# Kernel optimization log

Hardware: AMD Instinct MI355X
Metric: run time of the kernel (lower is better)

The kernel has to match this reference:

```python
import jax, jax.numpy as jnp
import numpy as np

N_NODES = 20000
N_EDGES = 320000
NFEAT = 50
ALPHA = 0.2  # leaky relu slope
EPS = 1e-16


def _gat_head(x, src, dst, W, a, concat):
    # x: (N, Fin), W: (Fin, Fout), a: (2*Fout,)
    N = x.shape[0]
    Wh = x @ W                      # (N, Fout)
    Fout = W.shape[1]
    # edge_h @ a == Wh[src] @ a[:Fout] + Wh[dst] @ a[Fout:]
    s_src = Wh @ a[:Fout]           # (N,)
    s_dst = Wh @ a[Fout:]           # (N,)
    e = jax.nn.leaky_relu(s_src[src] + s_dst[dst], negative_slope=ALPHA)  # (E,)
    # segment softmax over incoming edges of each target node
    e_max = jax.ops.segment_max(e, dst, num_segments=N)   # (N,)
    e_exp = jnp.exp(e - e_max[dst])                         # (E,)
    e_sum = jax.ops.segment_sum(e_exp, dst, num_segments=N)
    att = e_exp / (e_sum[dst] + EPS)                        # (E,)
    msg = Wh[src] * att[:, None]                            # (E, Fout)
    h = jax.ops.segment_sum(msg, dst, num_segments=N)       # (N, Fout)
    return jax.nn.elu(h) if concat else h


def _multi_head(x, src, dst, W, a, concat):
    # W: (H, Fin, Fout), a: (H, 2*Fout) -> (H, N, Fout)
    return jax.vmap(_gat_head, in_axes=(None, None, None, 0, 0, None))(x, src, dst, W, a, concat)


def setup_inputs() -> dict:
    key = jax.random.key(0)
    ks = jax.random.split(key, 8)
    x = jax.random.normal(ks[0], (N_NODES, NFEAT), dtype=jnp.float32)
    edge_index = jax.random.randint(ks[1], (2, N_EDGES), 0, N_NODES, dtype=jnp.int64)
    s = 0.1
    W1 = jax.random.normal(ks[2], (4, NFEAT, 256), dtype=jnp.float32) * s
    a1 = jax.random.normal(ks[3], (4, 512), dtype=jnp.float32) * s
    W2 = jax.random.normal(ks[4], (4, 1024, 256), dtype=jnp.float32) * s
    a2 = jax.random.normal(ks[5], (4, 512), dtype=jnp.float32) * s
    W3 = jax.random.normal(ks[6], (6, 1024, 121), dtype=jnp.float32) * s
    a3 = jax.random.normal(ks[7], (6, 242), dtype=jnp.float32) * s
    return {"x": x, "edge_index": edge_index, "W1": W1, "a1": a1, "W2": W2, "a2": a2, "W3": W3, "a3": a3}


def reference(x, edge_index, W1, a1, W2, a2, W3, a3):
    src, dst = edge_index[0], edge_index[1]
    N = x.shape[0]
    # layer 1: 4 heads, concat -> (N, 1024), then elu
    h1 = _multi_head(x, src, dst, W1, a1, True)      # (4, N, 256)
    x1 = jnp.transpose(h1, (1, 0, 2)).reshape(N, -1)  # concat along feature dim
    x1 = jax.nn.elu(x1)
    # layer 2: 4 heads, concat + skip connection, then elu
    h2 = _multi_head(x1, src, dst, W2, a2, True)
    x2 = jnp.transpose(h2, (1, 0, 2)).reshape(N, -1)
    x2 = jax.nn.elu(x2 + x1)
    # layer 3: 6 heads, no concat-elu, mean over heads
    h3 = _multi_head(x2, src, dst, W3, a3, False)     # (6, N, 121)
    x3 = jnp.mean(h3, axis=0)
    return jax.nn.sigmoid(x3)
```

## Files before the change

kernel.cpp:

```cpp
#include <hip/hip_runtime.h>
#include <cstdint>

#define N_NODES 20000
#define N_EDGES 320000
#define ALPHA 0.2f
#define GAT_EPS 1e-16f
#define MPAD 20096
#define RBLK 157
#define RHI 20
#define SCAN_BLKS 80
#define BT_ROWS 1152

typedef __attribute__((ext_vector_type(8))) _Float16 half8;
typedef __attribute__((ext_vector_type(4))) _Float16 half4t;
typedef __attribute__((ext_vector_type(16))) float f32x16;
typedef __attribute__((ext_vector_type(2))) float f32x2;

__device__ __forceinline__ float elu1(float x) { return x > 0.f ? x : __expf(x) - 1.f; }

__device__ __forceinline__ unsigned char f2fp8(float x) {
    return (unsigned char)(__builtin_amdgcn_cvt_pk_fp8_f32(x, 0.f, 0, false) & 0xff);
}

__device__ __forceinline__ void async16(const void* g, void* l) {
    __builtin_amdgcn_global_load_lds(
        (const __attribute__((address_space(1))) unsigned int*)g,
        (__attribute__((address_space(3))) unsigned int*)l, 16, 0, 0);
}

__global__ void hist_kernel(const int* __restrict__ dst, int* __restrict__ counts, int E) {
    int e = blockIdx.x * blockDim.x + threadIdx.x;
    if (e < E) atomicAdd(&counts[dst[e]], 1);
}

__global__ void scan1_kernel(const int* __restrict__ counts, int* __restrict__ excl,
                             int* __restrict__ partial, int N) {
    __shared__ int sh[256];
    int t = threadIdx.x, b = blockIdx.x;
    int i = b * 256 + t;
    int v = (i < N) ? counts[i] : 0;
    sh[t] = v;
    __syncthreads();
    for (int d = 1; d < 256; d <<= 1) {
        int x = (t >= d) ? sh[t - d] : 0;
        __syncthreads();
        sh[t] += x;
        __syncthreads();
    }
    if (i < N) excl[i] = sh[t] - v;
    if (t == 255) partial[b] = sh[255];
}

__global__ void scan2_kernel(int* __restrict__ partial) {
    __shared__ int sh[128];
    int t = threadIdx.x;
    int v = (t < SCAN_BLKS) ? partial[t] : 0;
    sh[t] = v;
    __syncthreads();
    for (int d = 1; d < 128; d <<= 1) {
        int x = (t >= d) ? sh[t - d] : 0;
        __syncthreads();
        sh[t] += x;
        __syncthreads();
    }
    if (t < SCAN_BLKS) partial[t] = sh[t] - v;
}

__global__ void scan3_kernel(const int* __restrict__ excl, const int* __restrict__ partial,
                             int* __restrict__ rowptr, int* __restrict__ cursor, int N, int E) {
    int t = threadIdx.x, b = blockIdx.x;
    int i = b * 256 + t;
    if (i < N) {
        int v = excl[i] + partial[b];
        rowptr[i] = v;
        cursor[i] = v;
    }
    if (i == 0) rowptr[N] = E;
}

__global__ void scatter_kernel(const int* __restrict__ src, const int* __restrict__ dst,
                               int* __restrict__ cursor, int* __restrict__ esrc, int E) {
    int e = blockIdx.x * blockDim.x + threadIdx.x;
    if (e < E) {
        int p = atomicAdd(&cursor[dst[e]], 1);
        esrc[p] = src[e];
    }
}

__global__ void pack_x16(const float* __restrict__ x, _Float16* __restrict__ A) {
    int idx = blockIdx.x * 256 + threadIdx.x;
    int r = idx >> 6, c = idx & 63;
    float v = (r < N_NODES && c < 50) ? x[r * 50 + c] : 0.f;
    A[idx] = (_Float16)v;
}

__global__ void pack_bt1(const float* __restrict__ W, _Float16* __restrict__ Bt) {
    int idx = blockIdx.x * 256 + threadIdx.x;
    int c = idx >> 6, k = idx & 63;
    int h = c >> 8, f = c & 255;
    float v = (k < 50) ? W[((size_t)h * 50 + k) * 256 + f] : 0.f;
    Bt[idx] = (_Float16)v;
}

__global__ void pack_bt16(const float* __restrict__ W, _Float16* __restrict__ Bt,
                          int F, int Fpad, int Ctot) {
    int c = blockIdx.y;
    int k = blockIdx.x * blockDim.x + threadIdx.x;
    float v = 0.f;
    if (c < Ctot) {
        int h = c / Fpad, f = c - h * Fpad;
        if (f < F) v = W[(size_t)h * 1024 * F + (size_t)k * F + f];
    }
    Bt[(size_t)c * 1024 + k] = (_Float16)v;
}

__global__ __launch_bounds__(64) void wtilde_kernel(const float* __restrict__ W,
                                                    const float* __restrict__ a,
                                                    _Float16* __restrict__ BT, int Kreal,
                                                    int Kdim, int F, int H, int Nfeat) {
    int k = blockIdx.x, j = blockIdx.y;
    if (j >= 2 * H) return;
    int lane = threadIdx.x;
    int h = j < H ? j : j - H;
    int ao = j < H ? 0 : F;
    float s = 0.f;
    if (k < Kreal) {
        const float* wp = W + ((size_t)h * Kreal + k) * F;
        const float* ap = a + (size_t)h * 2 * F + ao;
        for (int f = lane; f < F; f += 64) s += wp[f] * ap[f];
    }
#pragma unroll
    for (int off = 32; off; off >>= 1) s += __shfl_down(s, off);
    if (lane == 0) BT[(size_t)(Nfeat + j) * Kdim + k] = (_Float16)s;
}

__global__ __launch_bounds__(256) void gemm_f16(const _Float16* __restrict__ A,
                                                const _Float16* __restrict__ BT,
                                                unsigned char* __restrict__ C8,
                                                float* __restrict__ SPRE,
                                                int M, int Nfeat, int ld, int Kdim, int Cblk) {
    int id = blockIdx.x;
    int xm = id & 7, q = id >> 3;
    int cb = q % Cblk, rh = q / Cblk;
    int rb = rh * 8 + xm;
    if (rb >= RBLK) return;
    __shared__ __align__(16) _Float16 sA[128 * 64];
    __shared__ __align__(16) _Float16 sB[128 * 64];
    int t = threadIdx.x;
    int row0 = rb * 128, col0 = cb * 128;
    int lane = t & 63, wave = t >> 6;
    int wm = wave >> 1, wn = wave & 1;
    int l31 = lane & 31;
    int lhi = lane >> 5;

    const _Float16* gA = A + (size_t)row0 * Kdim;
    const _Float16* gB = BT + (size_t)col0 * Kdim;

    int sR[4], sgl[4];
#pragma unroll
    for (int i = 0; i < 4; i++) {
        int m = i * 256 + t;
        sR[i] = m >> 3;
        sgl[i] = (m & 7) ^ (sR[i] & 7);
    }

    f32x16 acc[2][2] = {};

    for (int k0 = 0; k0 < Kdim; k0 += 64) {
        __syncthreads();
#pragma unroll
        for (int i = 0; i < 4; i++) {
            const _Float16* pa = gA + (size_t)sR[i] * Kdim + k0 + sgl[i] * 8;
            const _Float16* pb = gB + (size_t)sR[i] * Kdim + k0 + sgl[i] * 8;
            async16(pa, sA + (i * 256 + t) * 8);
            async16(pb, sB + (i * 256 + t) * 8);
        }
        __syncthreads();
#pragma unroll
        for (int kk = 0; kk < 4; kk++) {
            int g = kk * 2 + lhi;
            half8 af[2], bf[2];
#pragma unroll
            for (int mt = 0; mt < 2; mt++) {
                int R = wm * 64 + mt * 32 + l31;
                int gp = g ^ (R & 7);
                af[mt] = *(const half8*)(sA + R * 64 + gp * 8);
            }
#pragma unroll
            for (int nt = 0; nt < 2; nt++) {
                int R = wn * 64 + nt * 32 + l31;
                int gp = g ^ (R & 7);
                bf[nt] = *(const half8*)(sB + R * 64 + gp * 8);
            }
#pragma unroll
            for (int mt = 0; mt < 2; mt++)
#pragma unroll
                for (int nt = 0; nt < 2; nt++)
                    acc[mt][nt] = __builtin_amdgcn_mfma_f32_32x32x16_f16(af[mt], bf[nt], acc[mt][nt], 0, 0, 0);
        }
    }

    int cb32 = col0 + wn * 64 + l31;
    int rb32 = row0 + wm * 64 + 4 * lhi;
#pragma unroll
    for (int mt = 0; mt < 2; mt++)
#pragma unroll
        for (int nt = 0; nt < 2; nt++) {
            int gc = cb32 + nt * 32;
            if (gc < Nfeat) {
#pragma unroll
                for (int r = 0; r < 16; r++) {
                    int gr = rb32 + mt * 32 + (r & 3) + 8 * (r >> 2);
                    if (gr < M) C8[(size_t)gr * ld + gc] = f2fp8(acc[mt][nt][r]);
                }
            } else if (gc < Nfeat + 12) {
                int j = gc - Nfeat;
#pragma unroll
                for (int r = 0; r < 16; r++) {
                    int gr = rb32 + mt * 32 + (r & 3) + 8 * (r >> 2);
                    if (gr < M) SPRE[(size_t)j * N_NODES + gr] = acc[mt][nt][r];
                }
            }
        }
}

__global__ void att_kernel(const int* __restrict__ rowptr,
                           const int* __restrict__ esrc,
                           const float* __restrict__ SS,
                           const float* __restrict__ SD,
                           float* __restrict__ ATT, int N, int H) {
    int n = blockIdx.x;
    int h = threadIdx.x >> 6;
    int lane = threadIdx.x & 63;
    if (h >= H) return;
    int start = rowptr[n], end = rowptr[n + 1];
    const float* ss = SS + (size_t)h * N;
    float sd = SD[(size_t)h * N + n];
    float* att = ATT + (size_t)h * N_EDGES;
    float m = -1e30f, s = 0.f;
    for (int e = start + lane; e < end; e += 64) {
        float sc = ss[esrc[e]] + sd;
        sc = sc > 0.f ? sc : ALPHA * sc;
        float mn = fmaxf(m, sc);
        s = s * __expf(m - mn) + __expf(sc - mn);
        m = mn;
    }
#pragma unroll
    for (int off = 1; off < 64; off <<= 1) {
        float mo = __shfl_xor(m, off);
        float so = __shfl_xor(s, off);
        float mn = fmaxf(m, mo);
        s = s * __expf(m - mn) + so * __expf(mo - mn);
        m = mn;
    }
    float inv = 1.f / (s + GAT_EPS);
    for (int e = start + lane; e < end; e += 64) {
        float sc = ss[esrc[e]] + sd;
        sc = sc > 0.f ? sc : ALPHA * sc;
        att[e] = __expf(sc - m) * inv;
    }
}

__global__ __launch_bounds__(64) void agg256_kernel(const unsigned char* __restrict__ WH8,
                                                    const int* __restrict__ rowptr,
                                                    const int* __restrict__ esrc,
                                                    const float* __restrict__ ATT,
                                                    _Float16* __restrict__ X16,
                                                    int use_skip, int N) {
    int id = blockIdx.x;
    int h = id & 3, n = id >> 2;
    int lane = threadIdx.x;
    int base = h * 256 + lane * 4;
    int start = rowptr[n], end = rowptr[n + 1];
    const float* ap = ATT + (size_t)h * N_EDGES;
    const unsigned char* W = WH8 + base;
    float a0 = 0.f, a1 = 0.f, a2 = 0.f, a3 = 0.f;
    int e = start;
    for (; e + 8 <= end; e += 8) {
#pragma unroll
        for (int u = 0; u < 8; u += 4) {
            int i0 = esrc[e + u], i1 = esrc[e + u + 1], i2 = esrc[e + u + 2], i3 = esrc[e + u + 3];
            float p0 = ap[e + u], p1 = ap[e + u + 1], p2 = ap[e + u + 2], p3 = ap[e + u + 3];
            unsigned int w0 = *(const unsigned int*)(W + (size_t)i0 * 1024);
            unsigned int w1 = *(const unsigned int*)(W + (size_t)i1 * 1024);
            unsigned int w2 = *(const unsigned int*)(W + (size_t)i2 * 1024);
            unsigned int w3 = *(const unsigned int*)(W + (size_t)i3 * 1024);
            f32x2 l0 = __builtin_amdgcn_cvt_pk_f32_fp8((int)w0, false);
            f32x2 h0v = __builtin_amdgcn_cvt_pk_f32_fp8((int)w0, true);
            f32x2 l1 = __builtin_amdgcn_cvt_pk_f32_fp8((int)w1, false);
            f32x2 h1v = __builtin_amdgcn_cvt_pk_f32_fp8((int)w1, true);
            f32x2 l2 = __builtin_amdgcn_cvt_pk_f32_fp8((int)w2, false);
            f32x2 h2v = __builtin_amdgcn_cvt_pk_f32_fp8((int)w2, true);
            f32x2 l3 = __builtin_amdgcn_cvt_pk_f32_fp8((int)w3, false);
            f32x2 h3v = __builtin_amdgcn_cvt_pk_f32_fp8((int)w3, true);
            a0 += p0 * l0.x + p1 * l1.x + p2 * l2.x + p3 * l3.x;
            a1 += p0 * l0.y + p1 * l1.y + p2 * l2.y + p3 * l3.y;
            a2 += p0 * h0v.x + p1 * h1v.x + p2 * h2v.x + p3 * h3v.x;
            a3 += p0 * h0v.y + p1 * h1v.y + p2 * h2v.y + p3 * h3v.y;
        }
    }
    for (; e < end; e++) {
        float p = ap[e];
        unsigned int w = *(const unsigned int*)(W + (size_t)esrc[e] * 1024);
        f32x2 lo = __builtin_amdgcn_cvt_pk_f32_fp8((int)w, false);
        f32x2 hi = __builtin_amdgcn_cvt_pk_f32_fp8((int)w, true);
        a0 += p * lo.x; a1 += p * lo.y; a2 += p * hi.x; a3 += p * hi.y;
    }
    size_t o = (size_t)n * 1024 + base;
    float v0, v1, v2, v3;
    if (use_skip) {
        half4t sk = *(const half4t*)(X16 + o);
        v0 = elu1(elu1(a0) + (float)sk.x);
        v1 = elu1(elu1(a1) + (float)sk.y);
        v2 = elu1(elu1(a2) + (float)sk.z);
        v3 = elu1(elu1(a3) + (float)sk.w);
    } else {
        v0 = elu1(elu1(a0)); v1 = elu1(elu1(a1));
        v2 = elu1(elu1(a2)); v3 = elu1(elu1(a3));
    }
    half4t r;
    r.x = (_Float16)v0; r.y = (_Float16)v1; r.z = (_Float16)v2; r.w = (_Float16)v3;
    *(half4t*)(X16 + o) = r;
}

__global__ __launch_bounds__(128) void agg726_kernel(const unsigned char* __restrict__ WH8,
                                                     const int* __restrict__ rowptr,
                                                     const int* __restrict__ esrc,
                                                     const float* __restrict__ ATT,
                                                     float* __restrict__ out, int N) {
    __shared__ float part[2][124];
    int t = threadIdx.x, n = blockIdx.x;
    int lane = t & 63, wv = t >> 6;
    int h0 = wv * 3;
    int start = rowptr[n], end = rowptr[n + 1];
    float acc[3][2] = {};
    if (lane < 62) {
        const unsigned char* W0 = WH8 + (h0 + 0) * 124 + 2 * lane;
        const unsigned char* W1 = WH8 + (h0 + 1) * 124 + 2 * lane;
        const unsigned char* W2 = WH8 + (h0 + 2) * 124 + 2 * lane;
        const float* ap0 = ATT + (size_t)(h0 + 0) * N_EDGES;
        const float* ap1 = ATT + (size_t)(h0 + 1) * N_EDGES;
        const float* ap2 = ATT + (size_t)(h0 + 2) * N_EDGES;
        int e = start;
        for (; e + 2 <= end; e += 2) {
            size_t sa = (size_t)esrc[e] * 768, sb = (size_t)esrc[e + 1] * 768;
            float pa0 = ap0[e], pa1 = ap1[e], pa2 = ap2[e];
            float pb0 = ap0[e + 1], pb1 = ap1[e + 1], pb2 = ap2[e + 1];
            unsigned short wa0 = *(const unsigned short*)(W0 + sa);
            unsigned short wa1 = *(const unsigned short*)(W1 + sa);
            unsigned short wa2 = *(const unsigned short*)(W2 + sa);
            unsigned short wb0 = *(const unsigned short*)(W0 + sb);
            unsigned short wb1 = *(const unsigned short*)(W1 + sb);
            unsigned short wb2 = *(const unsigned short*)(W2 + sb);
            f32x2 fa0 = __builtin_amdgcn_cvt_pk_f32_fp8((int)wa0, false);
            f32x2 fa1 = __builtin_amdgcn_cvt_pk_f32_fp8((int)wa1, false);
            f32x2 fa2 = __builtin_amdgcn_cvt_pk_f32_fp8((int)wa2, false);
            f32x2 fb0 = __builtin_amdgcn_cvt_pk_f32_fp8((int)wb0, false);
            f32x2 fb1 = __builtin_amdgcn_cvt_pk_f32_fp8((int)wb1, false);
            f32x2 fb2 = __builtin_amdgcn_cvt_pk_f32_fp8((int)wb2, false);
            acc[0][0] += pa0 * fa0.x + pb0 * fb0.x;
            acc[0][1] += pa0 * fa0.y + pb0 * fb0.y;
            acc[1][0] += pa1 * fa1.x + pb1 * fb1.x;
            acc[1][1] += pa1 * fa1.y + pb1 * fb1.y;
            acc[2][0] += pa2 * fa2.x + pb2 * fb2.x;
            acc[2][1] += pa2 * fa2.y + pb2 * fb2.y;
        }
        for (; e < end; e++) {
            size_t sa = (size_t)esrc[e] * 768;
            float p0 = ap0[e], p1 = ap1[e], p2 = ap2[e];
            f32x2 f0 = __builtin_amdgcn_cvt_pk_f32_fp8((int)*(const unsigned short*)(W0 + sa), false);
            f32x2 f1 = __builtin_amdgcn_cvt_pk_f32_fp8((int)*(const unsigned short*)(W1 + sa), false);
            f32x2 f2 = __builtin_amdgcn_cvt_pk_f32_fp8((int)*(const unsigned short*)(W2 + sa), false);
            acc[0][0] += p0 * f0.x; acc[0][1] += p0 * f0.y;
            acc[1][0] += p1 * f1.x; acc[1][1] += p1 * f1.y;
            acc[2][0] += p2 * f2.x; acc[2][1] += p2 * f2.y;
        }
        part[wv][2 * lane]     = acc[0][0] + acc[1][0] + acc[2][0];
        part[wv][2 * lane + 1] = acc[0][1] + acc[1][1] + acc[2][1];
    }
    __syncthreads();
    if (t < 121) {
        float tot = (part[0][t] + part[1][t]) * (1.f / 6.f);
        out[(size_t)n * 121 + t] = 1.f / (1.f + __expf(-tot));
    }
}

extern "C" void kernel_launch(void* const* d_in, const int* in_sizes, int n_in,
                              void* d_out, int out_size, void* d_ws, size_t ws_size,
                              hipStream_t stream) {
    const float* x  = (const float*)d_in[0];
    const int*   ei = (const int*)d_in[1];
    const float* W1 = (const float*)d_in[2];
    const float* a1 = (const float*)d_in[3];
    const float* W2 = (const float*)d_in[4];
    const float* a2 = (const float*)d_in[5];
    const float* W3 = (const float*)d_in[6];
    const float* a3 = (const float*)d_in[7];
    float* out = (float*)d_out;
    const int N = N_NODES, E = N_EDGES;
    const int* src = ei;
    const int* dst = ei + E;

    char* ws = (char*)d_ws;
    size_t off = 0;
    auto alloc = [&](size_t b) { size_t o = off; off += (b + 255) & ~(size_t)255; return o; };
    _Float16* X16  = (_Float16*)(ws + alloc((size_t)MPAD * 1024 * 2));
    unsigned char* WH8 = (unsigned char*)(ws + alloc((size_t)MPAD * 1024));
    _Float16* BT16 = (_Float16*)(ws + alloc((size_t)BT_ROWS * 1024 * 2));
    _Float16* A1   = (_Float16*)(ws + alloc((size_t)MPAD * 64 * 2));
    _Float16* BT1  = (_Float16*)(ws + alloc((size_t)BT_ROWS * 64 * 2));
    float* SPRE   = (float*)(ws + alloc((size_t)12 * N * 4));
    float* ATT    = (float*)(ws + alloc((size_t)6 * E * 4));
    int*   rowptr = (int*)(ws + alloc((size_t)(N + 1) * 4));
    int*   cursor = (int*)(ws + alloc((size_t)N * 4));
    int*   counts = (int*)(ws + alloc((size_t)N * 4));
    int*   excl   = (int*)(ws + alloc((size_t)N * 4));
    int*   partial= (int*)(ws + alloc((size_t)SCAN_BLKS * 4));
    int*   esrc   = (int*)(ws + alloc((size_t)E * 4));

    hipMemsetAsync(counts, 0, (size_t)N * 4, stream);
    hist_kernel<<<(E + 255) / 256, 256, 0, stream>>>(dst, counts, E);
    scan1_kernel<<<SCAN_BLKS, 256, 0, stream>>>(counts, excl, partial, N);
    scan2_kernel<<<1, 128, 0, stream>>>(partial);
    scan3_kernel<<<SCAN_BLKS, 256, 0, stream>>>(excl, partial, rowptr, cursor, N, E);
    scatter_kernel<<<(E + 255) / 256, 256, 0, stream>>>(src, dst, cursor, esrc, E);
    hipMemsetAsync(X16 + (size_t)N * 1024, 0, (size_t)(MPAD - N) * 1024 * 2, stream);

    pack_x16<<<MPAD * 64 / 256, 256, 0, stream>>>(x, A1);
    pack_bt1<<<1024 * 64 / 256, 256, 0, stream>>>(W1, BT1);
    wtilde_kernel<<<dim3(64, 8), 64, 0, stream>>>(W1, a1, BT1, 50, 64, 256, 4, 1024);
    gemm_f16<<<8 * RHI * 9, 256, 0, stream>>>(A1, BT1, WH8, SPRE, N, 1024, 1024, 64, 9);
    att_kernel<<<N, 256, 0, stream>>>(rowptr, esrc, SPRE, SPRE + 4 * N, ATT, N, 4);
    agg256_kernel<<<N * 4, 64, 0, stream>>>(WH8, rowptr, esrc, ATT, X16, 0, N);

    pack_bt16<<<dim3(4, 1024), 256, 0, stream>>>(W2, BT16, 256, 256, 1024);
    wtilde_kernel<<<dim3(1024, 8), 64, 0, stream>>>(W2, a2, BT16, 1024, 1024, 256, 4, 1024);
    gemm_f16<<<8 * RHI * 9, 256, 0, stream>>>(X16, BT16, WH8, SPRE, N, 1024, 1024, 1024, 9);
    att_kernel<<<N, 256, 0, stream>>>(rowptr, esrc, SPRE, SPRE + 4 * N, ATT, N, 4);
    agg256_kernel<<<N * 4, 64, 0, stream>>>(WH8, rowptr, esrc, ATT, X16, 1, N);

    pack_bt16<<<dim3(4, 744), 256, 0, stream>>>(W3, BT16, 121, 124, 744);
    wtilde_kernel<<<dim3(1024, 12), 64, 0, stream>>>(W3, a3, BT16, 1024, 1024, 121, 6, 744);
    gemm_f16<<<8 * RHI * 6, 256, 0, stream>>>(X16, BT16, WH8, SPRE, N, 744, 768, 1024, 6);
    att_kernel<<<N, 384, 0, stream>>>(rowptr, esrc, SPRE, SPRE + 6 * N, ATT, N, 6);
    agg726_kernel<<<N, 128, 0, stream>>>(WH8, rowptr, esrc, ATT, out, N);
}
```

Baseline: 478.4 us.

## Fuse attention softmax into aggregation and double-buffer GEMM LDS tiles

Merges the per-node softmax kernel and the aggregation kernel for all three layers into one kernel. Each wave computes its head's scores, broadcasts the edge indices and weights with readlane, and accumulates the gathered fp8 features, so the ATT edge buffer is no longer written and read back. The GEMM also gains double-buffered LDS with a prefetch of the next K tile issued before compute, removing one barrier per iteration. The risks are the doubled LDS footprint in the GEMM and fewer blocks in the layer-2 aggregation (one block per node instead of one per node and head), which can reduce occupancy. The GEMM prefetch also depends on the barrier at the top of each iteration to keep the async LDS loads and reads in order.

```diff
diff --git a/kernel.cpp b/kernel.cpp
--- a/kernel.cpp
+++ b/kernel.cpp
@@ -26,6 +26,10 @@
     __builtin_amdgcn_global_load_lds(
         (const __attribute__((address_space(1))) unsigned int*)g,
         (__attribute__((address_space(3))) unsigned int*)l, 16, 0, 0);
+}
+
+__device__ __forceinline__ float rdlanef(float v, int j) {
+    return __int_as_float(__builtin_amdgcn_readlane(__float_as_int(v), j));
 }
 
 __global__ void hist_kernel(const int* __restrict__ dst, int* __restrict__ counts, int E) {
@@ -144,8 +148,8 @@
     int cb = q % Cblk, rh = q / Cblk;
     int rb = rh * 8 + xm;
     if (rb >= RBLK) return;
-    __shared__ __align__(16) _Float16 sA[128 * 64];
-    __shared__ __align__(16) _Float16 sB[128 * 64];
+    __shared__ __align__(16) _Float16 sA[2][128 * 64];
+    __shared__ __align__(16) _Float16 sB[2][128 * 64];
     int t = threadIdx.x;
     int row0 = rb * 128, col0 = cb * 128;
     int lane = t & 63, wave = t >> 6;
@@ -166,16 +170,30 @@
 
     f32x16 acc[2][2] = {};
 
+#pragma unroll
+    for (int i = 0; i < 4; i++) {
+        const _Float16* pa = gA + (size_t)sR[i] * Kdim + sgl[i] * 8;
+        const _Float16* pb = gB + (size_t)sR[i] * Kdim + sgl[i] * 8;
+        async16(pa, &sA[0][(i * 256 + t) * 8]);
+        async16(pb, &sB[0][(i * 256 + t) * 8]);
+    }
+
+    int cur = 0;
     for (int k0 = 0; k0 < Kdim; k0 += 64) {
         __syncthreads();
-#pragma unroll
-        for (int i = 0; i < 4; i++) {
-            const _Float16* pa = gA + (size_t)sR[i] * Kdim + k0 + sgl[i] * 8;
-            const _Float16* pb = gB + (size_t)sR[i] * Kdim + k0 + sgl[i] * 8;
-            async16(pa, sA + (i * 256 + t) * 8);
-            async16(pb, sB + (i * 256 + t) * 8);
-        }
-        __syncthreads();
+        int nxt = k0 + 64;
+        if (nxt < Kdim) {
+            int nb = cur ^ 1;
+#pragma unroll
+            for (int i = 0; i < 4; i++) {
+                const _Float16* pa = gA + (size_t)sR[i] * Kdim + nxt + sgl[i] * 8;
+                const _Float16* pb = gB + (size_t)sR[i] * Kdim + nxt + sgl[i] * 8;
+                async16(pa, &sA[nb][(i * 256 + t) * 8]);
+                async16(pb, &sB[nb][(i * 256 + t) * 8]);
+            }
+        }
+        const _Float16* cA = sA[cur];
+        const _Float16* cB = sB[cur];
 #pragma unroll
         for (int kk = 0; kk < 4; kk++) {
             int g = kk * 2 + lhi;
@@ -184,13 +202,13 @@
             for (int mt = 0; mt < 2; mt++) {
                 int R = wm * 64 + mt * 32 + l31;
                 int gp = g ^ (R & 7);
-                af[mt] = *(const half8*)(sA + R * 64 + gp * 8);
+                af[mt] = *(const half8*)(cA + R * 64 + gp * 8);
             }
 #pragma unroll
             for (int nt = 0; nt < 2; nt++) {
                 int R = wn * 64 + nt * 32 + l31;
                 int gp = g ^ (R & 7);
-                bf[nt] = *(const half8*)(sB + R * 64 + gp * 8);
+                bf[nt] = *(const half8*)(cB + R * 64 + gp * 8);
             }
 #pragma unroll
             for (int mt = 0; mt < 2; mt++)
@@ -198,6 +216,7 @@
                 for (int nt = 0; nt < 2; nt++)
                     acc[mt][nt] = __builtin_amdgcn_mfma_f32_32x32x16_f16(af[mt], bf[nt], acc[mt][nt], 0, 0, 0);
         }
+        cur ^= 1;
     }
 
     int cb32 = col0 + wn * 64 + l31;
@@ -224,25 +243,33 @@
         }
 }
 
-__global__ void att_kernel(const int* __restrict__ rowptr,
-                           const int* __restrict__ esrc,
-                           const float* __restrict__ SS,
-                           const float* __restrict__ SD,
-                           float* __restrict__ ATT, int N, int H) {
+__global__ __launch_bounds__(256) void attagg256_kernel(const int* __restrict__ rowptr,
+                                                        const int* __restrict__ esrc,
+                                                        const float* __restrict__ SPRE,
+                                                        const unsigned char* __restrict__ WH8,
+                                                        _Float16* __restrict__ X16,
+                                                        int use_skip, int N) {
     int n = blockIdx.x;
     int h = threadIdx.x >> 6;
     int lane = threadIdx.x & 63;
-    if (h >= H) return;
     int start = rowptr[n], end = rowptr[n + 1];
-    const float* ss = SS + (size_t)h * N;
-    float sd = SD[(size_t)h * N + n];
-    float* att = ATT + (size_t)h * N_EDGES;
+    const float* ss = SPRE + (size_t)h * N;
+    float sd = SPRE[(size_t)(4 + h) * N + n];
+
     float m = -1e30f, s = 0.f;
-    for (int e = start + lane; e < end; e += 64) {
-        float sc = ss[esrc[e]] + sd;
-        sc = sc > 0.f ? sc : ALPHA * sc;
+    int sidx = 0; float ssc = -1e30f;
+    for (int e0 = start; e0 < end; e0 += 64) {
+        int e = e0 + lane;
+        bool act = e < end;
+        int idx = act ? esrc[e] : 0;
+        float sc = -1e30f;
+        if (act) {
+            sc = ss[idx] + sd;
+            sc = sc > 0.f ? sc : ALPHA * sc;
+        }
+        sidx = idx; ssc = sc;
         float mn = fmaxf(m, sc);
-        s = s * __expf(m - mn) + __expf(sc - mn);
+        s = s * __expf(m - mn) + (act ? __expf(sc - mn) : 0.f);
         m = mn;
     }
 #pragma unroll
@@ -254,37 +281,37 @@
         m = mn;
     }
     float inv = 1.f / (s + GAT_EPS);
-    for (int e = start + lane; e < end; e += 64) {
-        float sc = ss[esrc[e]] + sd;
-        sc = sc > 0.f ? sc : ALPHA * sc;
-        att[e] = __expf(sc - m) * inv;
-    }
-}
-
-__global__ __launch_bounds__(64) void agg256_kernel(const unsigned char* __restrict__ WH8,
-                                                    const int* __restrict__ rowptr,
-                                                    const int* __restrict__ esrc,
-                                                    const float* __restrict__ ATT,
-                                                    _Float16* __restrict__ X16,
-                                                    int use_skip, int N) {
-    int id = blockIdx.x;
-    int h = id & 3, n = id >> 2;
-    int lane = threadIdx.x;
-    int base = h * 256 + lane * 4;
-    int start = rowptr[n], end = rowptr[n + 1];
-    const float* ap = ATT + (size_t)h * N_EDGES;
-    const unsigned char* W = WH8 + base;
+
+    const unsigned char* Wb = WH8 + h * 256 + lane * 4;
     float a0 = 0.f, a1 = 0.f, a2 = 0.f, a3 = 0.f;
-    int e = start;
-    for (; e + 8 <= end; e += 8) {
-#pragma unroll
-        for (int u = 0; u < 8; u += 4) {
-            int i0 = esrc[e + u], i1 = esrc[e + u + 1], i2 = esrc[e + u + 2], i3 = esrc[e + u + 3];
-            float p0 = ap[e + u], p1 = ap[e + u + 1], p2 = ap[e + u + 2], p3 = ap[e + u + 3];
-            unsigned int w0 = *(const unsigned int*)(W + (size_t)i0 * 1024);
-            unsigned int w1 = *(const unsigned int*)(W + (size_t)i1 * 1024);
-            unsigned int w2 = *(const unsigned int*)(W + (size_t)i2 * 1024);
-            unsigned int w3 = *(const unsigned int*)(W + (size_t)i3 * 1024);
+    int lastStart = start + (((end - start - 1) >> 6) << 6);
+    for (int e0 = start; e0 < end; e0 += 64) {
+        int e = e0 + lane;
+        bool act = e < end;
+        int idx; float sc;
+        if (e0 == lastStart) { idx = sidx; sc = ssc; }
+        else {
+            idx = act ? esrc[e] : 0;
+            sc = -1e30f;
+            if (act) {
+                sc = ss[idx] + sd;
+                sc = sc > 0.f ? sc : ALPHA * sc;
+            }
+        }
+        float p = act ? __expf(sc - m) * inv : 0.f;
+        int cnt = end - e0; if (cnt > 64) cnt = 64;
+        int j = 0;
+        for (; j + 4 <= cnt; j += 4) {
+            int i0 = __builtin_amdgcn_readlane(idx, j);
+            int i1 = __builtin_amdgcn_readlane(idx, j + 1);
+            int i2 = __builtin_amdgcn_readlane(idx, j + 2);
+            int i3 = __builtin_amdgcn_readlane(idx, j + 3);
+            float p0 = rdlanef(p, j), p1 = rdlanef(p, j + 1);
+            float p2 = rdlanef(p, j + 2), p3 = rdlanef(p, j + 3);
+            unsigned int w0 = *(const unsigned int*)(Wb + (size_t)i0 * 1024);
+            unsigned int w1 = *(const unsigned int*)(Wb + (size_t)i1 * 1024);
+            unsigned int w2 = *(const unsigned int*)(Wb + (size_t)i2 * 1024);
+            unsigned int w3 = *(const unsigned int*)(Wb + (size_t)i3 * 1024);
             f32x2 l0 = __builtin_amdgcn_cvt_pk_f32_fp8((int)w0, false);
             f32x2 h0v = __builtin_amdgcn_cvt_pk_f32_fp8((int)w0, true);
             f32x2 l1 = __builtin_amdgcn_cvt_pk_f32_fp8((int)w1, false);
@@ -298,15 +325,17 @@
             a2 += p0 * h0v.x + p1 * h1v.x + p2 * h2v.x + p3 * h3v.x;
             a3 += p0 * h0v.y + p1 * h1v.y + p2 * h2v.y + p3 * h3v.y;
         }
-    }
-    for (; e < end; e++) {
-        float p = ap[e];
-        unsigned int w = *(const unsigned int*)(W + (size_t)esrc[e] * 1024);
-        f32x2 lo = __builtin_amdgcn_cvt_pk_f32_fp8((int)w, false);
-        f32x2 hi = __builtin_amdgcn_cvt_pk_f32_fp8((int)w, true);
-        a0 += p * lo.x; a1 += p * lo.y; a2 += p * hi.x; a3 += p * hi.y;
-    }
-    size_t o = (size_t)n * 1024 + base;
+        for (; j < cnt; j++) {
+            int ij = __builtin_amdgcn_readlane(idx, j);
+            float pj = rdlanef(p, j);
+            unsigned int w = *(const unsigned int*)(Wb + (size_t)ij * 1024);
+            f32x2 lo = __builtin_amdgcn_cvt_pk_f32_fp8((int)w, false);
+            f32x2 hi = __builtin_amdgcn_cvt_pk_f32_fp8((int)w, true);
+            a0 += pj * lo.x; a1 += pj * lo.y; a2 += pj * hi.x; a3 += pj * hi.y;
+        }
+    }
+
+    size_t o = (size_t)n * 1024 + h * 256 + lane * 4;
     float v0, v1, v2, v3;
     if (use_skip) {
         half4t sk = *(const half4t*)(X16 + o);
@@ -323,64 +352,99 @@
     *(half4t*)(X16 + o) = r;
 }
 
-__global__ __launch_bounds__(128) void agg726_kernel(const unsigned char* __restrict__ WH8,
-                                                     const int* __restrict__ rowptr,
-                                                     const int* __restrict__ esrc,
-                                                     const float* __restrict__ ATT,
-                                                     float* __restrict__ out, int N) {
-    __shared__ float part[2][124];
-    int t = threadIdx.x, n = blockIdx.x;
-    int lane = t & 63, wv = t >> 6;
-    int h0 = wv * 3;
+__global__ __launch_bounds__(384) void attagg726_kernel(const int* __restrict__ rowptr,
+                                                        const int* __restrict__ esrc,
+                                                        const float* __restrict__ SPRE,
+                                                        const unsigned char* __restrict__ WH8,
+                                                        float* __restrict__ out, int N) {
+    __shared__ float part[6][124];
+    int n = blockIdx.x;
+    int t = threadIdx.x;
+    int h = t >> 6;
+    int lane = t & 63;
     int start = rowptr[n], end = rowptr[n + 1];
-    float acc[3][2] = {};
+    const float* ss = SPRE + (size_t)h * N;
+    float sd = SPRE[(size_t)(6 + h) * N + n];
+
+    float m = -1e30f, s = 0.f;
+    int sidx = 0; float ssc = -1e30f;
+    for (int e0 = start; e0 < end; e0 += 64) {
+        int e = e0 + lane;
+        bool act = e < end;
+        int idx = act ? esrc[e] : 0;
+        float sc = -1e30f;
+        if (act) {
+            sc = ss[idx] + sd;
+            sc = sc > 0.f ? sc : ALPHA * sc;
+        }
+        sidx = idx; ssc = sc;
+        float mn = fmaxf(m, sc);
+        s = s * __expf(m - mn) + (act ? __expf(sc - mn) : 0.f);
+        m = mn;
+    }
+#pragma unroll
+    for (int off = 1; off < 64; off <<= 1) {
+        float mo = __shfl_xor(m, off);
+        float so = __shfl_xor(s, off);
+        float mn = fmaxf(m, mo);
+        s = s * __expf(m - mn) + so * __expf(mo - mn);
+        m = mn;
+    }
+    float inv = 1.f / (s + GAT_EPS);
+
+    const unsigned char* Wb = WH8 + h * 124 + 2 * lane;
+    float a0 = 0.f, a1 = 0.f;
+    int lastStart = start + (((end - start - 1) >> 6) << 6);
+    for (int e0 = start; e0 < end; e0 += 64) {
+        int e = e0 + lane;
+        bool act = e < end;
+        int idx; float sc;
+        if (e0 == lastStart) { idx = sidx; sc = ssc; }
+        else {
+            idx = act ? esrc[e] : 0;
+            sc = -1e30f;
+            if (act) {
+                sc = ss[idx] + sd;
+                sc = sc > 0.f ? sc : ALPHA * sc;
+            }
+        }
+        float p = act ? __expf(sc - m) * inv : 0.f;
+        int cnt = end - e0; if (cnt > 64) cnt = 64;
+        int j = 0;
+        for (; j + 4 <= cnt; j += 4) {
+            int i0 = __builtin_amdgcn_readlane(idx, j);
+            int i1 = __builtin_amdgcn_readlane(idx, j + 1);
+            int i2 = __builtin_amdgcn_readlane(idx, j + 2);
+            int i3 = __builtin_amdgcn_readlane(idx, j + 3);
+            float p0 = rdlanef(p, j), p1 = rdlanef(p, j + 1);
+            float p2 = rdlanef(p, j + 2), p3 = rdlanef(p, j + 3);
+            unsigned short w0 = *(const unsigned short*)(Wb + (size_t)i0 * 768);
+            unsigned short w1 = *(const unsigned short*)(Wb + (size_t)i1 * 768);
+            unsigned short w2 = *(const unsigned short*)(Wb + (size_t)i2 * 768);
+            unsigned short w3 = *(const unsigned short*)(Wb + (size_t)i3 * 768);
+            f32x2 f0 = __builtin_amdgcn_cvt_pk_f32_fp8((int)w0, false);
+            f32x2 f1 = __builtin_amdgcn_cvt_pk_f32_fp8((int)w1, false);
+            f32x2 f2 = __builtin_amdgcn_cvt_pk_f32_fp8((int)w2, false);
+            f32x2 f3 = __builtin_amdgcn_cvt_pk_f32_fp8((int)w3, false);
+            a0 += p0 * f0.x + p1 * f1.x + p2 * f2.x + p3 * f3.x;
+            a1 += p0 * f0.y + p1 * f1.y + p2 * f2.y + p3 * f3.y;
+        }
+        for (; j < cnt; j++) {
+            int ij = __builtin_amdgcn_readlane(idx, j);
+            float pj = rdlanef(p, j);
+            unsigned short w = *(const unsigned short*)(Wb + (size_t)ij * 768);
+            f32x2 f = __builtin_amdgcn_cvt_pk_f32_fp8((int)w, false);
+            a0 += pj * f.x; a1 += pj * f.y;
+        }
+    }
     if (lane < 62) {
-        const unsigned char* W0 = WH8 + (h0 + 0) * 124 + 2 * lane;
-        const unsigned char* W1 = WH8 + (h0 + 1) * 124 + 2 * lane;
-        const unsigned char* W2 = WH8 + (h0 + 2) * 124 + 2 * lane;
-        const float* ap0 = ATT + (size_t)(h0 + 0) * N_EDGES;
-        const float* ap1 = ATT + (size_t)(h0 + 1) * N_EDGES;
-        const float* ap2 = ATT + (size_t)(h0 + 2) * N_EDGES;
-        int e = start;
-        for (; e + 2 <= end; e += 2) {
-            size_t sa = (size_t)esrc[e] * 768, sb = (size_t)esrc[e + 1] * 768;
-            float pa0 = ap0[e], pa1 = ap1[e], pa2 = ap2[e];
-            float pb0 = ap0[e + 1], pb1 = ap1[e + 1], pb2 = ap2[e + 1];
-            unsigned short wa0 = *(const unsigned short*)(W0 + sa);
-            unsigned short wa1 = *(const unsigned short*)(W1 + sa);
-            unsigned short wa2 = *(const unsigned short*)(W2 + sa);
-            unsigned short wb0 = *(const unsigned short*)(W0 + sb);
-            unsigned short wb1 = *(const unsigned short*)(W1 + sb);
-            unsigned short wb2 = *(const unsigned short*)(W2 + sb);
-            f32x2 fa0 = __builtin_amdgcn_cvt_pk_f32_fp8((int)wa0, false);
-            f32x2 fa1 = __builtin_amdgcn_cvt_pk_f32_fp8((int)wa1, false);
-            f32x2 fa2 = __builtin_amdgcn_cvt_pk_f32_fp8((int)wa2, false);
-            f32x2 fb0 = __builtin_amdgcn_cvt_pk_f32_fp8((int)wb0, false);
-            f32x2 fb1 = __builtin_amdgcn_cvt_pk_f32_fp8((int)wb1, false);
-            f32x2 fb2 = __builtin_amdgcn_cvt_pk_f32_fp8((int)wb2, false);
-            acc[0][0] += pa0 * fa0.x + pb0 * fb0.x;
-            acc[0][1] += pa0 * fa0.y + pb0 * fb0.y;
-            acc[1][0] += pa1 * fa1.x + pb1 * fb1.x;
-            acc[1][1] += pa1 * fa1.y + pb1 * fb1.y;
-            acc[2][0] += pa2 * fa2.x + pb2 * fb2.x;
-            acc[2][1] += pa2 * fa2.y + pb2 * fb2.y;
-        }
-        for (; e < end; e++) {
-            size_t sa = (size_t)esrc[e] * 768;
-            float p0 = ap0[e], p1 = ap1[e], p2 = ap2[e];
-            f32x2 f0 = __builtin_amdgcn_cvt_pk_f32_fp8((int)*(const unsigned short*)(W0 + sa), false);
-            f32x2 f1 = __builtin_amdgcn_cvt_pk_f32_fp8((int)*(const unsigned short*)(W1 + sa), false);
-            f32x2 f2 = __builtin_amdgcn_cvt_pk_f32_fp8((int)*(const unsigned short*)(W2 + sa), false);
-            acc[0][0] += p0 * f0.x; acc[0][1] += p0 * f0.y;
-            acc[1][0] += p1 * f1.x; acc[1][1] += p1 * f1.y;
-            acc[2][0] += p2 * f2.x; acc[2][1] += p2 * f2.y;
-        }
-        part[wv][2 * lane]     = acc[0][0] + acc[1][0] + acc[2][0];
-        part[wv][2 * lane + 1] = acc[0][1] + acc[1][1] + acc[2][1];
+        part[h][2 * lane]     = a0;
+        part[h][2 * lane + 1] = a1;
     }
     __syncthreads();
     if (t < 121) {
-        float tot = (part[0][t] + part[1][t]) * (1.f / 6.f);
+        float tot = (part[0][t] + part[1][t] + part[2][t] +
+                     part[3][t] + part[4][t] + part[5][t]) * (1.f / 6.f);
         out[(size_t)n * 121 + t] = 1.f / (1.f + __expf(-tot));
     }
 }
@@ -410,7 +474,6 @@
     _Float16* A1   = (_Float16*)(ws + alloc((size_t)MPAD * 64 * 2));
     _Float16* BT1  = (_Float16*)(ws + alloc((size_t)BT_ROWS * 64 * 2));
     float* SPRE   = (float*)(ws + alloc((size_t)12 * N * 4));
-    float* ATT    = (float*)(ws + alloc((size_t)6 * E * 4));
     int*   rowptr = (int*)(ws + alloc((size_t)(N + 1) * 4));
     int*   cursor = (int*)(ws + alloc((size_t)N * 4));
     int*   counts = (int*)(ws + alloc((size_t)N * 4));
@@ -430,18 +493,15 @@
     pack_bt1<<<1024 * 64 / 256, 256, 0, stream>>>(W1, BT1);
     wtilde_kernel<<<dim3(64, 8), 64, 0, stream>>>(W1, a1, BT1, 50, 64, 256, 4, 1024);
     gemm_f16<<<8 * RHI * 9, 256, 0, stream>>>(A1, BT1, WH8, SPRE, N, 1024, 1024, 64, 9);
-    att_kernel<<<N, 256, 0, stream>>>(rowptr, esrc, SPRE, SPRE + 4 * N, ATT, N, 4);
-    agg256_kernel<<<N * 4, 64, 0, stream>>>(WH8, rowptr, esrc, ATT, X16, 0, N);
+    attagg256_kernel<<<N, 256, 0, stream>>>(rowptr, esrc, SPRE, WH8, X16, 0, N);
 
     pack_bt16<<<dim3(4, 1024), 256, 0, stream>>>(W2, BT16, 256, 256, 1024);
     wtilde_kernel<<<dim3(1024, 8), 64, 0, stream>>>(W2, a2, BT16, 1024, 1024, 256, 4, 1024);
     gemm_f16<<<8 * RHI * 9, 256, 0, stream>>>(X16, BT16, WH8, SPRE, N, 1024, 1024, 1024, 9);
-    att_kernel<<<N, 256, 0, stream>>>(rowptr, esrc, SPRE, SPRE + 4 * N, ATT, N, 4);
-    agg256_kernel<<<N * 4, 64, 0, stream>>>(WH8, rowptr, esrc, ATT, X16, 1, N);
+    attagg256_kernel<<<N, 256, 0, stream>>>(rowptr, esrc, SPRE, WH8, X16, 1, N);
 
     pack_bt16<<<dim3(4, 744), 256, 0, stream>>>(W3, BT16, 121, 124, 744);
     wtilde_kernel<<<dim3(1024, 12), 64, 0, stream>>>(W3, a3, BT16, 1024, 1024, 121, 6, 744);
     gemm_f16<<<8 * RHI * 6, 256, 0, stream>>>(X16, BT16, WH8, SPRE, N, 744, 768, 1024, 6);
-    att_kernel<<<N, 384, 0, stream>>>(rowptr, esrc, SPRE, SPRE + 6 * N, ATT, N, 6);
-    agg726_kernel<<<N, 128, 0, stream>>>(WH8, rowptr, esrc, ATT, out, N);
-}
+    attagg726_kernel<<<N, 384, 0, stream>>>(rowptr, esrc, SPRE, WH8, out, N);
+}
```

Result: faster. 462.5 us (-3.3%).
